# Performance work log

Measured on AMD Instinct MI355X. Metric: run time of the kernel, lower is better.

Reference implementation:

```python
import jax, jax.numpy as jnp
import numpy as np
import math

D_MODEL = 1024
NUM_HEADS = 16
D_K = D_MODEL // NUM_HEADS


def setup_inputs() -> dict:
    key = jax.random.key(0)
    ks = jax.random.split(key, 9)
    s = 1.0 / math.sqrt(D_MODEL)
    x = jax.random.normal(ks[0], (2, 2048, D_MODEL), dtype=jnp.float32)
    # torch Linear params: weight [out, in], bias [out]
    Wq = jax.random.uniform(ks[1], (D_MODEL, D_MODEL), jnp.float32, -s, s)
    bq = jax.random.uniform(ks[2], (D_MODEL,), jnp.float32, -s, s)
    Wk = jax.random.uniform(ks[3], (D_MODEL, D_MODEL), jnp.float32, -s, s)
    bk = jax.random.uniform(ks[4], (D_MODEL,), jnp.float32, -s, s)
    Wv = jax.random.uniform(ks[5], (D_MODEL, D_MODEL), jnp.float32, -s, s)
    bv = jax.random.uniform(ks[6], (D_MODEL,), jnp.float32, -s, s)
    Wo = jax.random.uniform(ks[7], (D_MODEL, D_MODEL), jnp.float32, -s, s)
    bo = jax.random.uniform(ks[8], (D_MODEL,), jnp.float32, -s, s)
    return {"x": x, "Wq": Wq, "bq": bq, "Wk": Wk, "bk": bk,
            "Wv": Wv, "bv": bv, "Wo": Wo, "bo": bo}


def reference(x, Wq, bq, Wk, bk, Wv, bv, Wo, bo):
    B, T, _ = x.shape
    scale = 1.0 / math.sqrt(D_MODEL)  # NOTE: module scales by sqrt(d_model), not sqrt(d_k)

    def proj(W, b):
        # torch Linear: x @ W^T + b, then split heads -> [B, H, T, d_k]
        y = jnp.einsum('btd,ed->bte', x, W) + b
        return y.reshape(B, T, NUM_HEADS, D_K).transpose(0, 2, 1, 3)

    Q = proj(Wq, bq)
    K = proj(Wk, bk)
    V = proj(Wv, bv)
    logits = jnp.einsum('bhtd,bhsd->bhts', Q, K) * scale  # [B,H,T,T]
    attn = jax.nn.softmax(logits, axis=-1)
    out = jnp.einsum('bhts,bhsd->bhtd', attn, V)  # [B,H,T,d_k]
    out = out.transpose(0, 2, 1, 3).reshape(B, T, D_MODEL)
    return jnp.einsum('btd,ed->bte', out, Wo) + bo
```

## Files before the change

kernel.cpp:

```cpp
#include <hip/hip_runtime.h>

#define T_SEQ 2048
#define NB 2
#define NH 16
#define DK 64
#define DMODEL 1024

typedef __bf16 bf16x8 __attribute__((ext_vector_type(8)));
typedef float f32x4 __attribute__((ext_vector_type(4)));
typedef unsigned short ushortx8 __attribute__((ext_vector_type(8)));
typedef unsigned short ushortx4 __attribute__((ext_vector_type(4)));

__device__ inline unsigned short f2b1(float f) {
  unsigned u = __float_as_uint(f);
  u += 0x7fffu + ((u >> 16) & 1u);
  return (unsigned short)(u >> 16);
}

__device__ inline void gload16(const void* g, void* l) {
  __builtin_amdgcn_global_load_lds((const __attribute__((address_space(1))) void*)g,
                                   (__attribute__((address_space(3))) void*)l, 16, 0, 0);
}

__device__ inline bf16x8 mk8(unsigned a, unsigned b, unsigned c, unsigned d) {
  uint4 t = {a, b, c, d};
  return *(bf16x8*)&t;
}

__global__ void prep(const float* __restrict__ x,
                     const float* __restrict__ w0, const float* __restrict__ w1,
                     const float* __restrict__ w2, const float* __restrict__ w3,
                     const float* __restrict__ bq, const float* __restrict__ bk,
                     const float* __restrict__ bv,
                     unsigned short* __restrict__ xb, unsigned short* __restrict__ Wqkv,
                     float* __restrict__ bqkv) {
  int bid = blockIdx.x, tid = threadIdx.x;
  if (bid < 4096) {
    int i = (bid * 256 + tid) * 4;
    float4 v = *(const float4*)(x + i);
    ushortx4 o;
    o.x = f2b1(v.x); o.y = f2b1(v.y); o.z = f2b1(v.z); o.w = f2b1(v.w);
    *(ushortx4*)(xb + i) = o;
  } else if (bid < 8192) {
    int which = (bid - 4096) >> 10;
    int i = (((bid - 4096) & 1023) * 256 + tid) * 4;
    const float* src = which == 0 ? w0 : which == 1 ? w1 : which == 2 ? w2 : w3;
    float4 v = *(const float4*)(src + i);
    ushortx4 o;
    o.x = f2b1(v.x); o.y = f2b1(v.y); o.z = f2b1(v.z); o.w = f2b1(v.w);
    *(ushortx4*)(Wqkv + (long)which * 1048576 + i) = o;
  } else {
    int i = (bid - 8192) * 256 + tid;
    if (i < 3072) {
      float v = (i < 1024) ? bq[i] : (i < 2048 ? bk[i - 1024] : bv[i - 2048]);
      bqkv[i] = v;
    }
  }
}

__global__ __launch_bounds__(256, 2)
void gemm_bt(const unsigned short* __restrict__ A, const unsigned short* __restrict__ B,
             const float* __restrict__ bias, unsigned short* __restrict__ Cb,
             float* __restrict__ Cf, int M, int N, int K, int scale_cols, float scl) {
  __shared__ unsigned short As[2][4096];
  __shared__ unsigned short Bs[2][4096];
  const int tid = threadIdx.x;
  const int w = tid >> 6, lane = tid & 63;
  const int quad = lane >> 4, l16 = lane & 15;
  const int bm = blockIdx.y, bn = blockIdx.x;
  const int wm = w >> 1, wn = w & 1;

  f32x4 acc[4][4] = {};

  const int srow = tid >> 2;
  const int c4 = tid & 3;
  const unsigned short* aG = A + (long)(bm * 128 + srow) * K + c4 * 8;
  const unsigned short* bG = B + (long)(bn * 128 + srow) * K + c4 * 8;
  const long rs64 = (long)64 * K;
  const int wo = w * 512;

  gload16(aG, As[0] + wo);
  gload16(aG + rs64, As[0] + 2048 + wo);
  gload16(bG, Bs[0] + wo);
  gload16(bG + rs64, Bs[0] + 2048 + wo);

  int buf = 0;
  for (int kt = 0; kt < K; kt += 32) {
    __syncthreads();
    {
      const int nb = buf ^ 1;
      gload16(aG + kt + 32, As[nb] + wo);
      gload16(aG + rs64 + kt + 32, As[nb] + 2048 + wo);
      gload16(bG + kt + 32, Bs[nb] + wo);
      gload16(bG + rs64 + kt + 32, Bs[nb] + 2048 + wo);
    }

    bf16x8 af[4], bfr[4];
#pragma unroll
    for (int mt = 0; mt < 4; mt++)
      af[mt] = *(const bf16x8*)(As[buf] + (wm * 64 + mt * 16 + l16) * 32 + quad * 8);
#pragma unroll
    for (int nt = 0; nt < 4; nt++)
      bfr[nt] = *(const bf16x8*)(Bs[buf] + (wn * 64 + nt * 16 + l16) * 32 + quad * 8);
#pragma unroll
    for (int mt = 0; mt < 4; mt++)
#pragma unroll
      for (int nt = 0; nt < 4; nt++)
        acc[mt][nt] = __builtin_amdgcn_mfma_f32_16x16x32_bf16(af[mt], bfr[nt], acc[mt][nt], 0, 0, 0);
    buf ^= 1;
  }

  const int col0 = bn * 128 + wn * 64 + l16;
#pragma unroll
  for (int mt = 0; mt < 4; mt++) {
    int row0 = bm * 128 + wm * 64 + mt * 16 + quad * 4;
#pragma unroll
    for (int nt = 0; nt < 4; nt++) {
      int col = col0 + nt * 16;
      float bb = bias[col];
      float s = (col < scale_cols) ? scl : 1.0f;
#pragma unroll
      for (int r = 0; r < 4; r++) {
        float v = (acc[mt][nt][r] + bb) * s;
        if (Cf) Cf[(long)(row0 + r) * N + col] = v;
        else    Cb[(long)(row0 + r) * N + col] = f2b1(v);
      }
    }
  }
}

__global__ __launch_bounds__(256)
void vtrans(const unsigned short* __restrict__ QKV, unsigned short* __restrict__ Vt) {
  __shared__ unsigned short tile[64 * 80];
  int tid = threadIdx.x;
  int b = blockIdx.y >> 4, h = blockIdx.y & 15, tt = blockIdx.x;
  const unsigned short* base = QKV + (long)(b * T_SEQ + tt * 64) * 3072 + 2048 + h * 64;
#pragma unroll
  for (int rr = 0; rr < 2; rr++) {
    int L = rr * 256 + tid;
    int row = L >> 3, c = L & 7;
    ushortx8 v = *(const ushortx8*)(base + (long)row * 3072 + c * 8);
    *(ushortx8*)(tile + row * 80 + c * 8) = v;
  }
  __syncthreads();
  unsigned short* obase = Vt + (long)((b * NH + h) * DK) * T_SEQ + tt * 64;
#pragma unroll
  for (int rr = 0; rr < 2; rr++) {
    int L = rr * 256 + tid;
    int d = L >> 3, c = L & 7;
    ushortx8 o;
#pragma unroll
    for (int j = 0; j < 8; j++) o[j] = tile[(c * 8 + j) * 80 + d];
    *(ushortx8*)(obase + (long)d * T_SEQ + c * 8) = o;
  }
}

__global__ __launch_bounds__(256, 4)
void attn3(const unsigned short* __restrict__ QKV, const unsigned short* __restrict__ Vt,
           float* __restrict__ Onum, float* __restrict__ Oden) {
  __shared__ unsigned short Ks[2][4096];
  __shared__ unsigned short Vs[2][4096];
  const int tid = threadIdx.x;
  const int w = tid >> 6, lane = tid & 63;
  const int quad = lane >> 4, l16 = lane & 15;

  const int id = blockIdx.x;
  const int group = (id & 7) | (((id >> 3) & 7) << 3);
  const int qt = id >> 6;
  const int bh = group >> 1, split = group & 1;
  const int b = bh >> 4, h = bh & 15;
  const long qkvBase = (long)b * T_SEQ * 3072;
  const int kv0 = split * 1024;

  bf16x8 qf[2][2];
#pragma unroll
  for (int g = 0; g < 2; g++) {
    const unsigned short* qp = QKV + qkvBase + (long)(qt * 128 + w * 32 + g * 16 + l16) * 3072 + h * 64 + quad * 8;
    qf[g][0] = *(const bf16x8*)qp;
    qf[g][1] = *(const bf16x8*)(qp + 32);
  }

  const unsigned short* kG[2];
  const unsigned short* vG[2];
#pragma unroll
  for (int i = 0; i < 2; i++) {
    int S = w * 128 + i * 64 + lane;
    int row = S >> 3;
    int c = (S & 7) ^ (row & 7);
    kG[i] = QKV + qkvBase + 1024 + h * 64 + (long)(kv0 + row) * 3072 + c * 8;
    vG[i] = Vt + (long)bh * DK * T_SEQ + (long)row * T_SEQ + kv0 + c * 8;
  }
  const int wo2 = w * 1024;

  gload16(kG[0], Ks[0] + wo2);
  gload16(kG[1], Ks[0] + wo2 + 512);
  gload16(vG[0], Vs[0] + wo2);
  gload16(vG[1], Vs[0] + wo2 + 512);
  kG[0] += 64 * 3072; kG[1] += 64 * 3072;
  vG[0] += 64;        vG[1] += 64;

  f32x4 acco[2][4] = {};
  float psum[2] = {0.f, 0.f};
  int buf = 0;
  const int e16 = (l16 & 7) * 16;

  for (int it = 0; it < 16; it++) {
    __syncthreads();
    {
      const int nb = buf ^ 1;
      gload16(kG[0], Ks[nb] + wo2);
      gload16(kG[1], Ks[nb] + wo2 + 512);
      gload16(vG[0], Vs[nb] + wo2);
      gload16(vG[1], Vs[nb] + wo2 + 512);
      kG[0] += 64 * 3072; kG[1] += 64 * 3072;
      vG[0] += 64;        vG[1] += 64;
    }

    f32x4 st[2][4];
#pragma unroll
    for (int nt = 0; nt < 4; nt++) {
      const char* kr = (char*)(Ks[buf]) + (nt * 16 + l16) * 128;
      bf16x8 k0 = *(const bf16x8*)(kr + ((quad * 16) ^ e16));
      bf16x8 k1 = *(const bf16x8*)(kr + (((quad + 4) * 16) ^ e16));
#pragma unroll
      for (int g = 0; g < 2; g++) {
        f32x4 z = {};
        z = __builtin_amdgcn_mfma_f32_16x16x32_bf16(k0, qf[g][0], z, 0, 0, 0);
        z = __builtin_amdgcn_mfma_f32_16x16x32_bf16(k1, qf[g][1], z, 0, 0, 0);
        st[g][nt] = z;
      }
    }

    bf16x8 pa[2][2];
#pragma unroll
    for (int g = 0; g < 2; g++) {
      unsigned pk[4][2];
#pragma unroll
      for (int nt = 0; nt < 4; nt++) {
        float p0 = __builtin_amdgcn_exp2f(st[g][nt][0]);
        float p1 = __builtin_amdgcn_exp2f(st[g][nt][1]);
        float p2 = __builtin_amdgcn_exp2f(st[g][nt][2]);
        float p3 = __builtin_amdgcn_exp2f(st[g][nt][3]);
        psum[g] += (p0 + p1) + (p2 + p3);
        unsigned a0 = __float_as_uint(p0) + 0x8000u;
        unsigned a1 = __float_as_uint(p1) + 0x8000u;
        unsigned a2 = __float_as_uint(p2) + 0x8000u;
        unsigned a3 = __float_as_uint(p3) + 0x8000u;
        pk[nt][0] = __builtin_amdgcn_perm(a1, a0, 0x07060302u);
        pk[nt][1] = __builtin_amdgcn_perm(a3, a2, 0x07060302u);
      }
      pa[g][0] = mk8(pk[0][0], pk[0][1], pk[1][0], pk[1][1]);
      pa[g][1] = mk8(pk[2][0], pk[2][1], pk[3][0], pk[3][1]);
    }

    const int off8 = (quad & 1) * 8;
    const int cq = quad >> 1;
#pragma unroll
    for (int nt = 0; nt < 4; nt++) {
      const char* vr = (char*)(Vs[buf]) + (nt * 16 + l16) * 128;
#pragma unroll
      for (int km = 0; km < 2; km++) {
        uint2 lo = *(const uint2*)(vr + (((km * 4 + cq) * 16) ^ e16) + off8);
        uint2 hi = *(const uint2*)(vr + (((km * 4 + cq + 2) * 16) ^ e16) + off8);
        bf16x8 vf = mk8(lo.x, lo.y, hi.x, hi.y);
#pragma unroll
        for (int g = 0; g < 2; g++)
          acco[g][nt] = __builtin_amdgcn_mfma_f32_16x16x32_bf16(pa[g][km], vf, acco[g][nt], 0, 0, 0);
      }
    }
    buf ^= 1;
  }

  const long rowBase = (long)bh * T_SEQ + qt * 128 + w * 32;
  const long numBase = ((long)split * 65536 + rowBase) * 64;
#pragma unroll
  for (int g = 0; g < 2; g++) {
    float v = psum[g];
    v += __shfl_xor(v, 16, 64);
    v += __shfl_xor(v, 32, 64);
    if (lane < 16)
      Oden[(long)split * 65536 + rowBase + g * 16 + lane] = v;
#pragma unroll
    for (int nt = 0; nt < 4; nt++)
#pragma unroll
      for (int r = 0; r < 4; r++)
        Onum[numBase + (long)(g * 16 + quad * 4 + r) * 64 + nt * 16 + l16] = acco[g][nt][r];
  }
}

__global__ __launch_bounds__(256)
void combine(const float* __restrict__ Onum, const float* __restrict__ Oden,
             unsigned short* __restrict__ Ob) {
  int idx = blockIdx.x * 256 + threadIdx.x;
  int rp = idx >> 4;
  int dq = (idx & 15) * 4;
  float4 n0 = *(const float4*)(Onum + (long)rp * 64 + dq);
  float4 n1 = *(const float4*)(Onum + 4194304L + (long)rp * 64 + dq);
  float den = Oden[rp] + Oden[65536 + rp];
  float rl = __builtin_amdgcn_rcpf(den);
  int bh = rp >> 11, t = rp & 2047;
  int b = bh >> 4, h = bh & 15;
  ushortx4 o;
  o.x = f2b1((n0.x + n1.x) * rl);
  o.y = f2b1((n0.y + n1.y) * rl);
  o.z = f2b1((n0.z + n1.z) * rl);
  o.w = f2b1((n0.w + n1.w) * rl);
  *(ushortx4*)(Ob + (long)(b * T_SEQ + t) * DMODEL + h * 64 + dq) = o;
}

extern "C" void kernel_launch(void* const* d_in, const int* in_sizes, int n_in,
                              void* d_out, int out_size, void* d_ws, size_t ws_size,
                              hipStream_t stream) {
  const float* x  = (const float*)d_in[0];
  const float* Wq = (const float*)d_in[1];
  const float* bq = (const float*)d_in[2];
  const float* Wk = (const float*)d_in[3];
  const float* bk = (const float*)d_in[4];
  const float* Wv = (const float*)d_in[5];
  const float* bv = (const float*)d_in[6];
  const float* Wo = (const float*)d_in[7];
  const float* bo = (const float*)d_in[8];
  float* out = (float*)d_out;

  unsigned short* xb   = (unsigned short*)d_ws;
  unsigned short* Wqkv = xb + 4194304;
  unsigned short* Wob  = Wqkv + 3145728;
  float*          bqkv = (float*)(Wob + 1048576);
  unsigned short* QKV  = (unsigned short*)(bqkv + 3072);
  unsigned short* Vt   = QKV + 12582912;
  unsigned short* Ob   = Vt + 4194304;
  float*          Onum = (float*)(Ob + 4194304);
  float*          Oden = Onum + 8388608;

  prep<<<8204, 256, 0, stream>>>(x, Wq, Wk, Wv, Wo, bq, bk, bv, xb, Wqkv, bqkv);

  gemm_bt<<<dim3(24, 32), 256, 0, stream>>>(xb, Wqkv, bqkv, QKV, nullptr,
                                            4096, 3072, 1024, 1024, 0.04508422037f);

  vtrans<<<dim3(32, 32), 256, 0, stream>>>(QKV, Vt);
  attn3<<<dim3(1024), 256, 0, stream>>>(QKV, Vt, Onum, Oden);
  combine<<<dim3(4096), 256, 0, stream>>>(Onum, Oden, Ob);

  gemm_bt<<<dim3(8, 32), 256, 0, stream>>>(Ob, Wob, bo, nullptr, out,
                                           4096, 1024, 1024, 0, 1.0f);
}
```

Baseline: 206.5 us.

## Fuse V transpose into QKV GEMM epilogue, bf16 partials, smaller out-proj tiles

The QKV projection GEMM now writes the V columns directly in transposed [b,h,d,t] layout, which removes the separate vtrans kernel and its extra read and write of V. The attention partial numerators are stored as bf16 instead of fp32, halving that traffic in attn3 and combine at some cost in accuracy. The output projection gets its own kernel with 64-row tiles and twice the blocks to improve occupancy, and the QKV GEMM launch bound is raised to 3 blocks per CU. Risks include strided 8-byte stores for V, bf16 rounding before the split combine, and register pressure under the tighter launch bound.

```diff
diff --git a/kernel.cpp b/kernel.cpp
--- a/kernel.cpp
+++ b/kernel.cpp
@@ -58,10 +58,10 @@
   }
 }
 
-__global__ __launch_bounds__(256, 2)
-void gemm_bt(const unsigned short* __restrict__ A, const unsigned short* __restrict__ B,
-             const float* __restrict__ bias, unsigned short* __restrict__ Cb,
-             float* __restrict__ Cf, int M, int N, int K, int scale_cols, float scl) {
+__global__ __launch_bounds__(256, 3)
+void gemm_qkv(const unsigned short* __restrict__ A, const unsigned short* __restrict__ B,
+              const float* __restrict__ bias, unsigned short* __restrict__ Cb,
+              unsigned short* __restrict__ Vt, int M, int N, int K, float scl) {
   __shared__ unsigned short As[2][4096];
   __shared__ unsigned short Bs[2][4096];
   const int tid = threadIdx.x;
@@ -111,6 +111,7 @@
   }
 
   const int col0 = bn * 128 + wn * 64 + l16;
+  const bool isV = (bn * 128) >= 2048;
 #pragma unroll
   for (int mt = 0; mt < 4; mt++) {
     int row0 = bm * 128 + wm * 64 + mt * 16 + quad * 4;
@@ -118,46 +119,93 @@
     for (int nt = 0; nt < 4; nt++) {
       int col = col0 + nt * 16;
       float bb = bias[col];
-      float s = (col < scale_cols) ? scl : 1.0f;
-#pragma unroll
-      for (int r = 0; r < 4; r++) {
-        float v = (acc[mt][nt][r] + bb) * s;
-        if (Cf) Cf[(long)(row0 + r) * N + col] = v;
-        else    Cb[(long)(row0 + r) * N + col] = f2b1(v);
+      float s = (col < 1024) ? scl : 1.0f;
+      if (!isV) {
+#pragma unroll
+        for (int r = 0; r < 4; r++)
+          Cb[(long)(row0 + r) * N + col] = f2b1((acc[mt][nt][r] + bb) * s);
+      } else {
+        int cv = col - 2048;
+        int h = cv >> 6, d = cv & 63;
+        int b = row0 >> 11, t0 = row0 & 2047;
+        ushortx4 o;
+        o.x = f2b1(acc[mt][nt][0] + bb);
+        o.y = f2b1(acc[mt][nt][1] + bb);
+        o.z = f2b1(acc[mt][nt][2] + bb);
+        o.w = f2b1(acc[mt][nt][3] + bb);
+        *(ushortx4*)(Vt + ((long)((b * NH + h) * DK + d)) * T_SEQ + t0) = o;
       }
     }
   }
 }
 
-__global__ __launch_bounds__(256)
-void vtrans(const unsigned short* __restrict__ QKV, unsigned short* __restrict__ Vt) {
-  __shared__ unsigned short tile[64 * 80];
-  int tid = threadIdx.x;
-  int b = blockIdx.y >> 4, h = blockIdx.y & 15, tt = blockIdx.x;
-  const unsigned short* base = QKV + (long)(b * T_SEQ + tt * 64) * 3072 + 2048 + h * 64;
-#pragma unroll
-  for (int rr = 0; rr < 2; rr++) {
-    int L = rr * 256 + tid;
-    int row = L >> 3, c = L & 7;
-    ushortx8 v = *(const ushortx8*)(base + (long)row * 3072 + c * 8);
-    *(ushortx8*)(tile + row * 80 + c * 8) = v;
-  }
-  __syncthreads();
-  unsigned short* obase = Vt + (long)((b * NH + h) * DK) * T_SEQ + tt * 64;
-#pragma unroll
-  for (int rr = 0; rr < 2; rr++) {
-    int L = rr * 256 + tid;
-    int d = L >> 3, c = L & 7;
-    ushortx8 o;
-#pragma unroll
-    for (int j = 0; j < 8; j++) o[j] = tile[(c * 8 + j) * 80 + d];
-    *(ushortx8*)(obase + (long)d * T_SEQ + c * 8) = o;
+__global__ __launch_bounds__(256, 2)
+void gemm_out(const unsigned short* __restrict__ A, const unsigned short* __restrict__ B,
+              const float* __restrict__ bias, float* __restrict__ Cf, int M, int N, int K) {
+  __shared__ unsigned short As[2][2048];
+  __shared__ unsigned short Bs[2][4096];
+  const int tid = threadIdx.x;
+  const int w = tid >> 6, lane = tid & 63;
+  const int quad = lane >> 4, l16 = lane & 15;
+  const int bm = blockIdx.y, bn = blockIdx.x;
+  const int wm = w >> 1, wn = w & 1;
+
+  f32x4 acc[2][4] = {};
+
+  const int srow = tid >> 2;
+  const int c4 = tid & 3;
+  const unsigned short* aG = A + (long)(bm * 64 + srow) * K + c4 * 8;
+  const unsigned short* bG = B + (long)(bn * 128 + srow) * K + c4 * 8;
+  const long rs64 = (long)64 * K;
+  const int wo = w * 512;
+
+  gload16(aG, As[0] + wo);
+  gload16(bG, Bs[0] + wo);
+  gload16(bG + rs64, Bs[0] + 2048 + wo);
+
+  int buf = 0;
+  for (int kt = 0; kt < K; kt += 32) {
+    __syncthreads();
+    {
+      const int nb = buf ^ 1;
+      gload16(aG + kt + 32, As[nb] + wo);
+      gload16(bG + kt + 32, Bs[nb] + wo);
+      gload16(bG + rs64 + kt + 32, Bs[nb] + 2048 + wo);
+    }
+
+    bf16x8 af[2], bfr[4];
+#pragma unroll
+    for (int mt = 0; mt < 2; mt++)
+      af[mt] = *(const bf16x8*)(As[buf] + (wm * 32 + mt * 16 + l16) * 32 + quad * 8);
+#pragma unroll
+    for (int nt = 0; nt < 4; nt++)
+      bfr[nt] = *(const bf16x8*)(Bs[buf] + (wn * 64 + nt * 16 + l16) * 32 + quad * 8);
+#pragma unroll
+    for (int mt = 0; mt < 2; mt++)
+#pragma unroll
+      for (int nt = 0; nt < 4; nt++)
+        acc[mt][nt] = __builtin_amdgcn_mfma_f32_16x16x32_bf16(af[mt], bfr[nt], acc[mt][nt], 0, 0, 0);
+    buf ^= 1;
+  }
+
+  const int col0 = bn * 128 + wn * 64 + l16;
+#pragma unroll
+  for (int mt = 0; mt < 2; mt++) {
+    int row0 = bm * 64 + wm * 32 + mt * 16 + quad * 4;
+#pragma unroll
+    for (int nt = 0; nt < 4; nt++) {
+      int col = col0 + nt * 16;
+      float bb = bias[col];
+#pragma unroll
+      for (int r = 0; r < 4; r++)
+        Cf[(long)(row0 + r) * N + col] = acc[mt][nt][r] + bb;
+    }
   }
 }
 
 __global__ __launch_bounds__(256, 4)
 void attn3(const unsigned short* __restrict__ QKV, const unsigned short* __restrict__ Vt,
-           float* __restrict__ Onum, float* __restrict__ Oden) {
+           unsigned short* __restrict__ Onum, float* __restrict__ Oden) {
   __shared__ unsigned short Ks[2][4096];
   __shared__ unsigned short Vs[2][4096];
   const int tid = threadIdx.x;
@@ -284,27 +332,27 @@
     for (int nt = 0; nt < 4; nt++)
 #pragma unroll
       for (int r = 0; r < 4; r++)
-        Onum[numBase + (long)(g * 16 + quad * 4 + r) * 64 + nt * 16 + l16] = acco[g][nt][r];
+        Onum[numBase + (long)(g * 16 + quad * 4 + r) * 64 + nt * 16 + l16] = f2b1(acco[g][nt][r]);
   }
 }
 
 __global__ __launch_bounds__(256)
-void combine(const float* __restrict__ Onum, const float* __restrict__ Oden,
+void combine(const unsigned short* __restrict__ Onum, const float* __restrict__ Oden,
              unsigned short* __restrict__ Ob) {
   int idx = blockIdx.x * 256 + threadIdx.x;
   int rp = idx >> 4;
   int dq = (idx & 15) * 4;
-  float4 n0 = *(const float4*)(Onum + (long)rp * 64 + dq);
-  float4 n1 = *(const float4*)(Onum + 4194304L + (long)rp * 64 + dq);
+  ushortx4 n0 = *(const ushortx4*)(Onum + (long)rp * 64 + dq);
+  ushortx4 n1 = *(const ushortx4*)(Onum + 4194304L + (long)rp * 64 + dq);
   float den = Oden[rp] + Oden[65536 + rp];
   float rl = __builtin_amdgcn_rcpf(den);
   int bh = rp >> 11, t = rp & 2047;
   int b = bh >> 4, h = bh & 15;
   ushortx4 o;
-  o.x = f2b1((n0.x + n1.x) * rl);
-  o.y = f2b1((n0.y + n1.y) * rl);
-  o.z = f2b1((n0.z + n1.z) * rl);
-  o.w = f2b1((n0.w + n1.w) * rl);
+  o.x = f2b1((__uint_as_float((unsigned)n0.x << 16) + __uint_as_float((unsigned)n1.x << 16)) * rl);
+  o.y = f2b1((__uint_as_float((unsigned)n0.y << 16) + __uint_as_float((unsigned)n1.y << 16)) * rl);
+  o.z = f2b1((__uint_as_float((unsigned)n0.z << 16) + __uint_as_float((unsigned)n1.z << 16)) * rl);
+  o.w = f2b1((__uint_as_float((unsigned)n0.w << 16) + __uint_as_float((unsigned)n1.w << 16)) * rl);
   *(ushortx4*)(Ob + (long)(b * T_SEQ + t) * DMODEL + h * 64 + dq) = o;
 }
 
@@ -329,18 +377,16 @@
   unsigned short* QKV  = (unsigned short*)(bqkv + 3072);
   unsigned short* Vt   = QKV + 12582912;
   unsigned short* Ob   = Vt + 4194304;
-  float*          Onum = (float*)(Ob + 4194304);
-  float*          Oden = Onum + 8388608;
+  unsigned short* Onum = Ob + 4194304;
+  float*          Oden = (float*)(Onum + 8388608);
 
   prep<<<8204, 256, 0, stream>>>(x, Wq, Wk, Wv, Wo, bq, bk, bv, xb, Wqkv, bqkv);
 
-  gemm_bt<<<dim3(24, 32), 256, 0, stream>>>(xb, Wqkv, bqkv, QKV, nullptr,
-                                            4096, 3072, 1024, 1024, 0.04508422037f);
-
-  vtrans<<<dim3(32, 32), 256, 0, stream>>>(QKV, Vt);
+  gemm_qkv<<<dim3(24, 32), 256, 0, stream>>>(xb, Wqkv, bqkv, QKV, Vt,
+                                             4096, 3072, 1024, 0.04508422037f);
+
   attn3<<<dim3(1024), 256, 0, stream>>>(QKV, Vt, Onum, Oden);
   combine<<<dim3(4096), 256, 0, stream>>>(Onum, Oden, Ob);
 
-  gemm_bt<<<dim3(8, 32), 256, 0, stream>>>(Ob, Wob, bo, nullptr, out,
-                                           4096, 1024, 1024, 0, 1.0f);
-}
+  gemm_out<<<dim3(8, 64), 256, 0, stream>>>(Ob, Wob, bo, out, 4096, 1024, 1024);
+}
```

Result: faster. 195.2 us (-5.5%).
